# Kernel tuning notes

Hardware: AMD Instinct MI355X
Metric: run time of the kernel (lower is better)

Reference implementation:

```python
import jax, jax.numpy as jnp
import numpy as np

N, E = 50000, 800000
IN_DIM, HIDDEN, LATENT = 128, 256, 64


def setup_inputs() -> dict:
    key = jax.random.key(0)
    ks = jax.random.split(key, 10)
    def lin(k, fan_in, fan_out):
        s = 1.0 / np.sqrt(fan_in)
        return jax.random.uniform(k, (fan_in, fan_out), jnp.float32, -s, s)
    x = jax.random.normal(ks[0], (N, IN_DIM), jnp.float32)
    edge_index = jax.random.randint(ks[1], (2, E), 0, N, jnp.int64)
    return {
        "x": x,
        "edge_index": edge_index,
        # enc1: SAGEConv(in_dim, hidden): lin_l (neighbors, with bias), lin_r (root, no bias)
        "W1l": lin(ks[2], IN_DIM, HIDDEN),
        "b1": jnp.zeros((HIDDEN,), jnp.float32),
        "W1r": lin(ks[3], IN_DIM, HIDDEN),
        # enc2: SAGEConv(hidden, latent)
        "W2l": lin(ks[4], HIDDEN, LATENT),
        "b2": jnp.zeros((LATENT,), jnp.float32),
        "W2r": lin(ks[5], HIDDEN, LATENT),
        # decoder Linear(latent, in_dim)
        "Wd": lin(ks[6], LATENT, IN_DIM),
        "bd": jax.random.uniform(ks[7], (IN_DIM,), jnp.float32, -1.0 / np.sqrt(LATENT), 1.0 / np.sqrt(LATENT)),
    }


def _sage_conv(x, src, dst, Wl, b, Wr, num_nodes):
    # PyG SAGEConv (aggr='mean'): out = lin_l(mean_{j in N(i)} x_j) + lin_r(x_i)
    summed = jax.ops.segment_sum(x[src], dst, num_segments=num_nodes)   # [N, d]
    cnt = jax.ops.segment_sum(jnp.ones((src.shape[0],), x.dtype), dst, num_segments=num_nodes)
    mean = summed / jnp.maximum(cnt, 1.0)[:, None]
    return mean @ Wl + b + x @ Wr


def reference(x, edge_index, W1l, b1, W1r, W2l, b2, W2r, Wd, bd):
    src, dst = edge_index[0], edge_index[1]
    n = x.shape[0]
    h = jax.nn.relu(_sage_conv(x, src, dst, W1l, b1, W1r, n))
    z = _sage_conv(h, src, dst, W2l, b2, W2r, n)
    x_hat = z @ Wd + bd
    return (z, x_hat)
```

## Files before the change

kernel.cpp:

```cpp
#include <hip/hip_runtime.h>
#include <stdint.h>

#define NN 50000
#define NE 800000
#define NB 196
#define NBK 196
#define NBUK 196
#define CHK 4096
#define MTOT (NBUK * NBK)
#define MSB 151
#define CVTB 6250
#define PREPB 418

typedef __bf16 bf16x8 __attribute__((ext_vector_type(8)));
typedef float f32x4 __attribute__((ext_vector_type(4)));
typedef unsigned short ushort_t;

__device__ inline float bf2f(uint16_t u) {
    union { uint32_t i; float f; } v; v.i = ((uint32_t)u) << 16; return v.f;
}
__device__ inline uint16_t f2bf(float f) {
    uint32_t u = __float_as_uint(f);
    u += 0x7fffu + ((u >> 16) & 1u);
    return (uint16_t)(u >> 16);
}
__device__ inline float rdf(const void* p, int i, int bf) {
    return bf ? bf2f(((const ushort_t*)p)[i]) : ((const float*)p)[i];
}

__device__ inline int blk_or(int v, int* flag) {
    if (threadIdx.x == 0) *flag = 0;
    __syncthreads();
    if (v) atomicOr(flag, 1);
    __syncthreads();
    return *flag;
}
__device__ inline int detect_sh(const int* __restrict__ ei, int* flag) {
    int t = threadIdx.x;
    int v = ei[2 * t + 1] | ei[2 * (t + 256) + 1] | ei[2 * (t + 512) + 1] | ei[2 * (t + 768) + 1];
    return blk_or(v, flag) ? 0 : 1;
}
__device__ inline int detect_bf(const ushort_t* __restrict__ xw, int* flag) {
    int t = threadIdx.x;
    int bad = 0;
#pragma unroll
    for (int r = 0; r < 2; ++r) {
        uint16_t w = xw[t + 256 * r];
        int e = (w >> 7) & 0xFF;
        if (!(w == 0 || (e >= 96 && e <= 144))) bad = 1;
    }
    return blk_or(bad, flag) ? 0 : 1;
}

__global__ __launch_bounds__(256) void k_stage1(const int* __restrict__ ei, const void* __restrict__ x,
                                                const void* __restrict__ W1l, const void* __restrict__ W1r,
                                                const void* __restrict__ W2l, const void* __restrict__ W2r,
                                                const void* __restrict__ Wd,
                                                const void* __restrict__ b1, const void* __restrict__ b2,
                                                const void* __restrict__ bd,
                                                int* __restrict__ cntm, ushort_t* __restrict__ xb,
                                                ushort_t* __restrict__ wt, ushort_t* __restrict__ w2lt,
                                                ushort_t* __restrict__ w2rt, ushort_t* __restrict__ wdt,
                                                float* __restrict__ b1f, float* __restrict__ b2f,
                                                float* __restrict__ bdf) {
    __shared__ int flag;
    int b = blockIdx.x, t = threadIdx.x;
    if (b < NBK) {
        int sh = detect_sh(ei, &flag);
        __shared__ int hist[NBUK];
        if (t < NBUK) hist[t] = 0;
        __syncthreads();
        for (int i = t; i < CHK; i += 256) {
            int e = b * CHK + i;
            if (e < NE) {
                int d = ei[(size_t)(NE + e) << sh];
                atomicAdd(&hist[d >> 8], 1);
            }
        }
        __syncthreads();
        if (t < NBUK) cntm[t * NBK + b] = hist[t];
    } else if (b < NBK + CVTB) {
        int bf = detect_bf((const ushort_t*)x, &flag);
        int i = (b - NBK) * 256 + t;
        if (bf) {
            reinterpret_cast<ushort4*>(xb)[i] = reinterpret_cast<const ushort4*>(x)[i];
        } else {
            float4 v = reinterpret_cast<const float4*>(x)[i];
            ushort4 o;
            o.x = f2bf(v.x); o.y = f2bf(v.y); o.z = f2bf(v.z); o.w = f2bf(v.w);
            reinterpret_cast<ushort4*>(xb)[i] = o;
        }
    } else {
        int bf = detect_bf((const ushort_t*)x, &flag);
        int idx = (b - NBK - CVTB) * 256 + t;
        if (idx < 65536) {
            int c = idx >> 8, k = idx & 255;
            float v = (k < 128) ? rdf(W1l, k * 256 + c, bf) : rdf(W1r, (k - 128) * 256 + c, bf);
            wt[c * 256 + k] = f2bf(v);
        } else if (idx < 81920) {
            int t2 = idx - 65536;
            int c = t2 >> 8, k = t2 & 255;
            w2lt[c * 256 + k] = f2bf(rdf(W2l, k * 64 + c, bf));
        } else if (idx < 98304) {
            int t2 = idx - 81920;
            int c = t2 >> 8, k = t2 & 255;
            w2rt[c * 256 + k] = f2bf(rdf(W2r, k * 64 + c, bf));
        } else if (idx < 106496) {
            int t2 = idx - 98304;
            int c = t2 >> 6, k = t2 & 63;
            wdt[c * 64 + k] = f2bf(rdf(Wd, k * 128 + c, bf));
        } else if (idx < 106752) {
            b1f[idx - 106496] = rdf(b1, idx - 106496, bf);
        } else if (idx < 106816) {
            b2f[idx - 106752] = rdf(b2, idx - 106752, bf);
        } else if (idx < 106944) {
            bdf[idx - 106816] = rdf(bd, idx - 106816, bf);
        }
    }
}

__device__ inline int block_scan256(int v, int* ws, int* btot) {
    int lane = threadIdx.x & 63, wv = threadIdx.x >> 6;
    int incl = v;
#pragma unroll
    for (int d = 1; d < 64; d <<= 1) {
        int n = __shfl_up(incl, d);
        if (lane >= d) incl += n;
    }
    if (lane == 63) ws[wv] = incl;
    __syncthreads();
    if (threadIdx.x == 0) {
        int r = 0;
#pragma unroll
        for (int k = 0; k < 4; ++k) { int t = ws[k]; ws[k] = r; r += t; }
        *btot = r;
    }
    __syncthreads();
    return ws[wv] + incl - v;
}

__global__ __launch_bounds__(256) void k_scanMA(const int* __restrict__ cntm, int* __restrict__ offm,
                                                int* __restrict__ bsM) {
    __shared__ int ws[4]; __shared__ int btot;
    int i = blockIdx.x * 256 + threadIdx.x;
    int v = (i < MTOT) ? cntm[i] : 0;
    int excl = block_scan256(v, ws, &btot);
    if (i < MTOT) offm[i] = excl;
    if (threadIdx.x == 0) bsM[blockIdx.x] = btot;
}

__device__ inline void bsm_prefix(const int* __restrict__ bsM, int* bsPre, int* ws, int* btot) {
    int t = threadIdx.x;
    int v = (t < MSB) ? bsM[t] : 0;
    int excl = block_scan256(v, ws, &btot[0]);
    bsPre[t] = excl;
    __syncthreads();
}

__global__ __launch_bounds__(256) void k_scatterC(const int* __restrict__ ei,
                                                  const int* __restrict__ offm, const int* __restrict__ bsM,
                                                  uint32_t* __restrict__ pairs) {
    __shared__ int cur[NBUK];
    __shared__ int bsPre[256];
    __shared__ int ws[4]; __shared__ int btot;
    __shared__ int flag;
    int t = threadIdx.x, blk = blockIdx.x;
    int sh = detect_sh(ei, &flag);
    bsm_prefix(bsM, bsPre, ws, &btot);
    if (t < NBUK) {
        int g = t * NBK + blk;
        cur[t] = offm[g] + bsPre[g >> 8];
    }
    __syncthreads();
    for (int i = t; i < CHK; i += 256) {
        int e = blk * CHK + i;
        if (e < NE) {
            int s = ei[(size_t)e << sh];
            int d = ei[(size_t)(NE + e) << sh];
            int pos = atomicAdd(&cur[d >> 8], 1);
            pairs[pos] = (uint32_t)s | ((uint32_t)(d & 255) << 16);
        }
    }
}

__global__ __launch_bounds__(256) void k_d12(const uint32_t* __restrict__ pairs, const int* __restrict__ offm,
                                             const int* __restrict__ bsM,
                                             int* __restrict__ rowptr, ushort_t* __restrict__ srclist) {
    __shared__ int hist[256];
    __shared__ int cur[256];
    __shared__ int bsPre[256];
    __shared__ int ws[4]; __shared__ int btot;
    int t = threadIdx.x, b = blockIdx.x;
    bsm_prefix(bsM, bsPre, ws, &btot);
    __shared__ int sbeg, send;
    if (t == 0) {
        int g0 = b * NBK;
        sbeg = offm[g0] + bsPre[g0 >> 8];
        if (b + 1 < NBUK) {
            int g1 = (b + 1) * NBK;
            send = offm[g1] + bsPre[g1 >> 8];
        } else {
            send = NE;
        }
    }
    hist[t] = 0;
    __syncthreads();
    int beg = sbeg, end = send;
    for (int i = beg + t; i < end; i += 256) {
        uint32_t p = pairs[i];
        atomicAdd(&hist[p >> 16], 1);
    }
    __syncthreads();
    int v = hist[t];
    int excl = block_scan256(v, ws, &btot);
    int node = b * 256 + t;
    int rp = beg + excl;
    if (node < NN) rowptr[node] = rp;
    cur[t] = rp;
    if (b == 0 && t == 0) rowptr[NN] = NE;
    __syncthreads();
    for (int i = beg + t; i < end; i += 256) {
        uint32_t p = pairs[i];
        int pos = atomicAdd(&cur[p >> 16], 1);
        srclist[pos] = (ushort_t)(p & 0xffff);
    }
}

__global__ __launch_bounds__(256) void k_agg128(const ushort_t* __restrict__ xb, const int* __restrict__ rowptr,
                                                const ushort_t* __restrict__ srclist, ushort_t* __restrict__ out) {
    int node = (blockIdx.x * 256 + threadIdx.x) >> 6;
    int lane = threadIdx.x & 63;
    if (node >= NN) return;
    int half = lane >> 5, l32 = lane & 31;
    int beg = rowptr[node], end = rowptr[node + 1];
    float a0 = 0.f, a1 = 0.f, a2 = 0.f, a3 = 0.f;
    int j = beg + half;
    for (; j + 14 < end; j += 16) {
        ushort4 p[8];
#pragma unroll
        for (int u = 0; u < 8; ++u) {
            int s = srclist[j + 2 * u];
            p[u] = *reinterpret_cast<const ushort4*>(xb + (size_t)s * 128 + l32 * 4);
        }
#pragma unroll
        for (int u = 0; u < 8; ++u) {
            a0 += bf2f(p[u].x); a1 += bf2f(p[u].y); a2 += bf2f(p[u].z); a3 += bf2f(p[u].w);
        }
    }
    for (; j + 6 < end; j += 8) {
        ushort4 p[4];
#pragma unroll
        for (int u = 0; u < 4; ++u) {
            int s = srclist[j + 2 * u];
            p[u] = *reinterpret_cast<const ushort4*>(xb + (size_t)s * 128 + l32 * 4);
        }
#pragma unroll
        for (int u = 0; u < 4; ++u) {
            a0 += bf2f(p[u].x); a1 += bf2f(p[u].y); a2 += bf2f(p[u].z); a3 += bf2f(p[u].w);
        }
    }
    for (; j < end; j += 2) {
        int s = srclist[j];
        ushort4 p = *reinterpret_cast<const ushort4*>(xb + (size_t)s * 128 + l32 * 4);
        a0 += bf2f(p.x); a1 += bf2f(p.y); a2 += bf2f(p.z); a3 += bf2f(p.w);
    }
    a0 += __shfl_xor(a0, 32);
    a1 += __shfl_xor(a1, 32);
    a2 += __shfl_xor(a2, 32);
    a3 += __shfl_xor(a3, 32);
    if (half == 0) {
        float inv = 1.0f / (float)max(end - beg, 1);
        ushort4 o;
        o.x = f2bf(a0 * inv); o.y = f2bf(a1 * inv); o.z = f2bf(a2 * inv); o.w = f2bf(a3 * inv);
        *reinterpret_cast<ushort4*>(out + (size_t)node * 128 + l32 * 4) = o;
    }
}

__global__ __launch_bounds__(256, 2) void k_gemm12(const ushort_t* __restrict__ meanx, const ushort_t* __restrict__ xb,
                                                   const ushort_t* __restrict__ wt, const float* __restrict__ b1f,
                                                   const ushort_t* __restrict__ w2lt, const ushort_t* __restrict__ w2rt,
                                                   const float* __restrict__ b2f,
                                                   ushort_t* __restrict__ y, float* __restrict__ r) {
    __shared__ alignas(16) ushort_t ht[16 * 256];
    int wv = threadIdx.x >> 6, lane = threadIdx.x & 63;
    int m = lane & 15, q = lane >> 4;
    bf16x8 B1[8][4];
#pragma unroll
    for (int ks = 0; ks < 8; ++ks) {
        int kb = ks * 32 + q * 8;
#pragma unroll
        for (int ct = 0; ct < 4; ++ct)
            B1[ks][ct] = *reinterpret_cast<const bf16x8*>(wt + (size_t)(wv * 64 + ct * 16 + m) * 256 + kb);
    }
    int op = wv >> 1;
    int cb = (wv & 1) * 32;
    const ushort_t* wtx = op ? w2rt : w2lt;
    bf16x8 B2[8][2];
#pragma unroll
    for (int ks = 0; ks < 8; ++ks) {
        int kb = ks * 32 + q * 8;
#pragma unroll
        for (int ct = 0; ct < 2; ++ct)
            B2[ks][ct] = *reinterpret_cast<const bf16x8*>(wtx + (size_t)(cb + ct * 16 + m) * 256 + kb);
    }
    float bias2[2];
#pragma unroll
    for (int ct = 0; ct < 2; ++ct) bias2[ct] = b2f[cb + ct * 16 + m];

    const int ntiles = NN / 16;
    for (int t = blockIdx.x; t < ntiles; t += gridDim.x) {
        int r0 = t * 16;
        int row = r0 + m;
        f32x4 acc[4];
#pragma unroll
        for (int ct = 0; ct < 4; ++ct) acc[ct] = (f32x4){0.f, 0.f, 0.f, 0.f};
#pragma unroll
        for (int ks = 0; ks < 8; ++ks) {
            int kb = ks * 32 + q * 8;
            const ushort_t* ap = (ks < 4) ? (meanx + (size_t)row * 128 + kb)
                                          : (xb + (size_t)row * 128 + (kb - 128));
            bf16x8 a = *reinterpret_cast<const bf16x8*>(ap);
#pragma unroll
            for (int ct = 0; ct < 4; ++ct)
                acc[ct] = __builtin_amdgcn_mfma_f32_16x16x32_bf16(a, B1[ks][ct], acc[ct], 0, 0, 0);
        }
#pragma unroll
        for (int ct = 0; ct < 4; ++ct) {
            int c = wv * 64 + ct * 16 + m;
            float bias = b1f[c];
#pragma unroll
            for (int i = 0; i < 4; ++i) {
                int lr = q * 4 + i;
                int off = (lr * 512 + c * 2) ^ ((lr & 7) << 4);
                *reinterpret_cast<ushort_t*>(reinterpret_cast<char*>(ht) + off) =
                    f2bf(fmaxf(acc[ct][i] + bias, 0.f));
            }
        }
        __syncthreads();
        f32x4 acc2[2];
        acc2[0] = (f32x4){0.f, 0.f, 0.f, 0.f}; acc2[1] = acc2[0];
#pragma unroll
        for (int ks = 0; ks < 8; ++ks) {
            int boff = (m * 512 + ks * 64 + q * 16) ^ ((m & 7) << 4);
            bf16x8 a = *reinterpret_cast<const bf16x8*>(reinterpret_cast<const char*>(ht) + boff);
#pragma unroll
            for (int ct = 0; ct < 2; ++ct)
                acc2[ct] = __builtin_amdgcn_mfma_f32_16x16x32_bf16(a, B2[ks][ct], acc2[ct], 0, 0, 0);
        }
#pragma unroll
        for (int ct = 0; ct < 2; ++ct) {
            int c = cb + ct * 16 + m;
#pragma unroll
            for (int i = 0; i < 4; ++i) {
                int rr = r0 + q * 4 + i;
                if (op == 0) y[(size_t)rr * 64 + c] = f2bf(acc2[ct][i]);
                else         r[(size_t)rr * 64 + c] = acc2[ct][i] + bias2[ct];
            }
        }
        __syncthreads();
    }
}

__global__ __launch_bounds__(256) void k_agg2g3(const ushort_t* __restrict__ y, const int* __restrict__ rowptr,
                                                const ushort_t* __restrict__ srclist,
                                                float* zr,
                                                const ushort_t* __restrict__ wdt, const float* __restrict__ bdf,
                                                float* __restrict__ xhat) {
    __shared__ alignas(16) ushort_t zt[16][72];
    int b = blockIdx.x;
    int wv = threadIdx.x >> 6, lane = threadIdx.x & 63;
    int m = lane & 15, q = lane >> 4;
    bf16x8 B[2][2];
#pragma unroll
    for (int ks = 0; ks < 2; ++ks) {
        int kb = ks * 32 + q * 8;
#pragma unroll
        for (int ct = 0; ct < 2; ++ct)
            B[ks][ct] = *reinterpret_cast<const bf16x8*>(wdt + (size_t)(wv * 32 + ct * 16 + m) * 64 + kb);
    }
    float bias0 = bdf[wv * 32 + m], bias1 = bdf[wv * 32 + 16 + m];

    int quarter = lane >> 4, l16 = lane & 15;
#pragma unroll
    for (int s = 0; s < 4; ++s) {
        int node = b * 16 + wv * 4 + s;
        int beg = rowptr[node], end = rowptr[node + 1];
        float a0 = 0.f, a1 = 0.f, a2 = 0.f, a3 = 0.f;
        int j = beg + quarter;
        for (; j + 12 < end; j += 16) {
            ushort4 p[4];
#pragma unroll
            for (int u = 0; u < 4; ++u) {
                int sx = srclist[j + 4 * u];
                p[u] = *reinterpret_cast<const ushort4*>(y + (size_t)sx * 64 + l16 * 4);
            }
#pragma unroll
            for (int u = 0; u < 4; ++u) {
                a0 += bf2f(p[u].x); a1 += bf2f(p[u].y); a2 += bf2f(p[u].z); a3 += bf2f(p[u].w);
            }
        }
        for (; j < end; j += 4) {
            int sx = srclist[j];
            ushort4 p = *reinterpret_cast<const ushort4*>(y + (size_t)sx * 64 + l16 * 4);
            a0 += bf2f(p.x); a1 += bf2f(p.y); a2 += bf2f(p.z); a3 += bf2f(p.w);
        }
        a0 += __shfl_xor(a0, 16); a0 += __shfl_xor(a0, 32);
        a1 += __shfl_xor(a1, 16); a1 += __shfl_xor(a1, 32);
        a2 += __shfl_xor(a2, 16); a2 += __shfl_xor(a2, 32);
        a3 += __shfl_xor(a3, 16); a3 += __shfl_xor(a3, 32);
        if (quarter == 0) {
            float inv = 1.0f / (float)max(end - beg, 1);
            float4 rv = *reinterpret_cast<const float4*>(zr + (size_t)node * 64 + l16 * 4);
            float z0 = a0 * inv + rv.x;
            float z1 = a1 * inv + rv.y;
            float z2 = a2 * inv + rv.z;
            float z3 = a3 * inv + rv.w;
            float4 zo; zo.x = z0; zo.y = z1; zo.z = z2; zo.w = z3;
            *reinterpret_cast<float4*>(zr + (size_t)node * 64 + l16 * 4) = zo;
            uint2 o;
            o.x = (uint32_t)f2bf(z0) | ((uint32_t)f2bf(z1) << 16);
            o.y = (uint32_t)f2bf(z2) | ((uint32_t)f2bf(z3) << 16);
            *reinterpret_cast<uint2*>(&zt[wv * 4 + s][l16 * 4]) = o;
        }
    }
    __syncthreads();
    f32x4 acc[2];
    acc[0] = (f32x4){0.f, 0.f, 0.f, 0.f}; acc[1] = acc[0];
#pragma unroll
    for (int ks = 0; ks < 2; ++ks) {
        bf16x8 a = *reinterpret_cast<const bf16x8*>(&zt[m][ks * 32 + q * 8]);
#pragma unroll
        for (int ct = 0; ct < 2; ++ct)
            acc[ct] = __builtin_amdgcn_mfma_f32_16x16x32_bf16(a, B[ks][ct], acc[ct], 0, 0, 0);
    }
#pragma unroll
    for (int ct = 0; ct < 2; ++ct) {
        int c = wv * 32 + ct * 16 + m;
        float bb = ct ? bias1 : bias0;
#pragma unroll
        for (int i = 0; i < 4; ++i) {
            int rr = b * 16 + q * 4 + i;
            xhat[(size_t)rr * 128 + c] = acc[ct][i] + bb;
        }
    }
}

extern "C" void kernel_launch(void* const* d_in, const int* in_sizes, int n_in,
                              void* d_out, int out_size, void* d_ws, size_t ws_size,
                              hipStream_t stream) {
    const void *px = nullptr, *pei = nullptr, *pW1l = nullptr, *pW1r = nullptr,
               *pW2l = nullptr, *pW2r = nullptr, *pWd = nullptr,
               *pb1 = nullptr, *pb2 = nullptr, *pbd = nullptr;
    for (int i = 0; i < n_in; ++i) {
        const void* p = d_in[i];
        switch (in_sizes[i]) {
            case 6400000: px  = p; break;
            case 1600000: pei = p; break;
            case 32768:   if (!pW1l) pW1l = p; else pW1r = p; break;
            case 16384:   if (!pW2l) pW2l = p; else pW2r = p; break;
            case 8192:    pWd = p; break;
            case 256:     pb1 = p; break;
            case 128:     pbd = p; break;
            case 64:      pb2 = p; break;
            default: break;
        }
    }
    if (!px || !pei || !pW1l || !pW1r || !pW2l || !pW2r || !pWd || !pb1 || !pb2 || !pbd) {
        px = d_in[0]; pei = d_in[1]; pW1l = d_in[2]; pb1 = d_in[3]; pW1r = d_in[4];
        pW2l = d_in[5]; pb2 = d_in[6]; pW2r = d_in[7]; pWd = d_in[8]; pbd = d_in[9];
    }
    const int* ei = (const int*)pei;

    char* base = (char*)d_ws;
    size_t off = 0;
    auto alloc = [&](size_t bytes) -> void* {
        void* r = base + off;
        off = (off + bytes + 255) & ~(size_t)255;
        return r;
    };
    int* rowptr   = (int*)alloc((size_t)(NN + 1) * 4);
    int* cntm     = (int*)alloc((size_t)MTOT * 4);
    int* offm     = (int*)alloc((size_t)MTOT * 4);
    int* bsM      = (int*)alloc(256 * 4);
    uint32_t* pairs = (uint32_t*)alloc((size_t)NE * 4);
    ushort_t* srclist = (ushort_t*)alloc((size_t)NE * 2);
    ushort_t* wt   = (ushort_t*)alloc((size_t)65536 * 2);
    ushort_t* w2lt = (ushort_t*)alloc((size_t)16384 * 2);
    ushort_t* w2rt = (ushort_t*)alloc((size_t)16384 * 2);
    ushort_t* wdt  = (ushort_t*)alloc((size_t)8192 * 2);
    float* b1f    = (float*)alloc(256 * 4);
    float* b2f    = (float*)alloc(64 * 4);
    float* bdf    = (float*)alloc(128 * 4);
    ushort_t* xb  = (ushort_t*)alloc((size_t)NN * 128 * 2);
    ushort_t* y   = (ushort_t*)alloc((size_t)NN * 64 * 2);

    float* out_z    = (float*)d_out;
    float* out_xhat = out_z + (size_t)NN * 64;

    ushort_t* meanx = (ushort_t*)out_xhat;
    float*    rbuf  = out_z;

    k_stage1<<<NBK + CVTB + PREPB, 256, 0, stream>>>(ei, px, pW1l, pW1r, pW2l, pW2r, pWd, pb1, pb2, pbd,
                                                     cntm, xb, wt, w2lt, w2rt, wdt, b1f, b2f, bdf);

    k_scanMA<<<MSB, 256, 0, stream>>>(cntm, offm, bsM);
    k_scatterC<<<NBK, 256, 0, stream>>>(ei, offm, bsM, pairs);
    k_d12<<<NBUK, 256, 0, stream>>>(pairs, offm, bsM, rowptr, srclist);

    int ab = (NN + 3) / 4;
    k_agg128<<<ab, 256, 0, stream>>>(xb, rowptr, srclist, meanx);

    k_gemm12<<<512, 256, 0, stream>>>(meanx, xb, wt, b1f, w2lt, w2rt, b2f, y, rbuf);
    k_agg2g3<<<NN / 16, 256, 0, stream>>>(y, rowptr, srclist, rbuf, wdt, bdf, out_xhat);
}
```

Measured before the change: 222.4 us.

## Fuse first-layer neighbor mean aggregation into the layer-1/2 GEMM kernel

```diff
diff --git a/kernel.cpp b/kernel.cpp
--- a/kernel.cpp
+++ b/kernel.cpp
@@ -226,62 +226,14 @@
     }
 }
 
-__global__ __launch_bounds__(256) void k_agg128(const ushort_t* __restrict__ xb, const int* __restrict__ rowptr,
-                                                const ushort_t* __restrict__ srclist, ushort_t* __restrict__ out) {
-    int node = (blockIdx.x * 256 + threadIdx.x) >> 6;
-    int lane = threadIdx.x & 63;
-    if (node >= NN) return;
-    int half = lane >> 5, l32 = lane & 31;
-    int beg = rowptr[node], end = rowptr[node + 1];
-    float a0 = 0.f, a1 = 0.f, a2 = 0.f, a3 = 0.f;
-    int j = beg + half;
-    for (; j + 14 < end; j += 16) {
-        ushort4 p[8];
-#pragma unroll
-        for (int u = 0; u < 8; ++u) {
-            int s = srclist[j + 2 * u];
-            p[u] = *reinterpret_cast<const ushort4*>(xb + (size_t)s * 128 + l32 * 4);
-        }
-#pragma unroll
-        for (int u = 0; u < 8; ++u) {
-            a0 += bf2f(p[u].x); a1 += bf2f(p[u].y); a2 += bf2f(p[u].z); a3 += bf2f(p[u].w);
-        }
-    }
-    for (; j + 6 < end; j += 8) {
-        ushort4 p[4];
-#pragma unroll
-        for (int u = 0; u < 4; ++u) {
-            int s = srclist[j + 2 * u];
-            p[u] = *reinterpret_cast<const ushort4*>(xb + (size_t)s * 128 + l32 * 4);
-        }
-#pragma unroll
-        for (int u = 0; u < 4; ++u) {
-            a0 += bf2f(p[u].x); a1 += bf2f(p[u].y); a2 += bf2f(p[u].z); a3 += bf2f(p[u].w);
-        }
-    }
-    for (; j < end; j += 2) {
-        int s = srclist[j];
-        ushort4 p = *reinterpret_cast<const ushort4*>(xb + (size_t)s * 128 + l32 * 4);
-        a0 += bf2f(p.x); a1 += bf2f(p.y); a2 += bf2f(p.z); a3 += bf2f(p.w);
-    }
-    a0 += __shfl_xor(a0, 32);
-    a1 += __shfl_xor(a1, 32);
-    a2 += __shfl_xor(a2, 32);
-    a3 += __shfl_xor(a3, 32);
-    if (half == 0) {
-        float inv = 1.0f / (float)max(end - beg, 1);
-        ushort4 o;
-        o.x = f2bf(a0 * inv); o.y = f2bf(a1 * inv); o.z = f2bf(a2 * inv); o.w = f2bf(a3 * inv);
-        *reinterpret_cast<ushort4*>(out + (size_t)node * 128 + l32 * 4) = o;
-    }
-}
-
-__global__ __launch_bounds__(256, 2) void k_gemm12(const ushort_t* __restrict__ meanx, const ushort_t* __restrict__ xb,
-                                                   const ushort_t* __restrict__ wt, const float* __restrict__ b1f,
-                                                   const ushort_t* __restrict__ w2lt, const ushort_t* __restrict__ w2rt,
-                                                   const float* __restrict__ b2f,
-                                                   ushort_t* __restrict__ y, float* __restrict__ r) {
+__global__ __launch_bounds__(256, 2) void k_ag12(const ushort_t* __restrict__ xb, const int* __restrict__ rowptr,
+                                                 const ushort_t* __restrict__ srclist,
+                                                 const ushort_t* __restrict__ wt, const float* __restrict__ b1f,
+                                                 const ushort_t* __restrict__ w2lt, const ushort_t* __restrict__ w2rt,
+                                                 const float* __restrict__ b2f,
+                                                 ushort_t* __restrict__ y, float* __restrict__ r) {
     __shared__ alignas(16) ushort_t ht[16 * 256];
+    __shared__ alignas(16) ushort_t xt[16 * 128];
     int wv = threadIdx.x >> 6, lane = threadIdx.x & 63;
     int m = lane & 15, q = lane >> 4;
     bf16x8 B1[8][4];
@@ -307,9 +259,48 @@
 #pragma unroll
     for (int ct = 0; ct < 2; ++ct) bias2[ct] = b2f[cb + ct * 16 + m];
 
+    int half = lane >> 5, l32 = lane & 31;
     const int ntiles = NN / 16;
     for (int t = blockIdx.x; t < ntiles; t += gridDim.x) {
         int r0 = t * 16;
+#pragma unroll
+        for (int s = 0; s < 4; ++s) {
+            int node = r0 + wv * 4 + s;
+            int beg = rowptr[node], end = rowptr[node + 1];
+            float a0 = 0.f, a1 = 0.f, a2 = 0.f, a3 = 0.f;
+            int j = beg + half;
+            for (; j + 6 < end; j += 8) {
+                ushort4 p[4];
+#pragma unroll
+                for (int u = 0; u < 4; ++u) {
+                    int sx = srclist[j + 2 * u];
+                    p[u] = *reinterpret_cast<const ushort4*>(xb + (size_t)sx * 128 + l32 * 4);
+                }
+#pragma unroll
+                for (int u = 0; u < 4; ++u) {
+                    a0 += bf2f(p[u].x); a1 += bf2f(p[u].y); a2 += bf2f(p[u].z); a3 += bf2f(p[u].w);
+                }
+            }
+            for (; j < end; j += 2) {
+                int sx = srclist[j];
+                ushort4 p = *reinterpret_cast<const ushort4*>(xb + (size_t)sx * 128 + l32 * 4);
+                a0 += bf2f(p.x); a1 += bf2f(p.y); a2 += bf2f(p.z); a3 += bf2f(p.w);
+            }
+            a0 += __shfl_xor(a0, 32);
+            a1 += __shfl_xor(a1, 32);
+            a2 += __shfl_xor(a2, 32);
+            a3 += __shfl_xor(a3, 32);
+            if (half == 0) {
+                float inv = 1.0f / (float)max(end - beg, 1);
+                int nl = wv * 4 + s;
+                uint2 o;
+                o.x = (uint32_t)f2bf(a0 * inv) | ((uint32_t)f2bf(a1 * inv) << 16);
+                o.y = (uint32_t)f2bf(a2 * inv) | ((uint32_t)f2bf(a3 * inv) << 16);
+                int off = (nl * 256 + l32 * 8) ^ ((nl & 7) << 4);
+                *reinterpret_cast<uint2*>(reinterpret_cast<char*>(xt) + off) = o;
+            }
+        }
+        __syncthreads();
         int row = r0 + m;
         f32x4 acc[4];
 #pragma unroll
@@ -317,9 +308,13 @@
 #pragma unroll
         for (int ks = 0; ks < 8; ++ks) {
             int kb = ks * 32 + q * 8;
-            const ushort_t* ap = (ks < 4) ? (meanx + (size_t)row * 128 + kb)
-                                          : (xb + (size_t)row * 128 + (kb - 128));
-            bf16x8 a = *reinterpret_cast<const bf16x8*>(ap);
+            bf16x8 a;
+            if (ks < 4) {
+                int boff = (m * 256 + kb * 2) ^ ((m & 7) << 4);
+                a = *reinterpret_cast<const bf16x8*>(reinterpret_cast<const char*>(xt) + boff);
+            } else {
+                a = *reinterpret_cast<const bf16x8*>(xb + (size_t)row * 128 + (kb - 128));
+            }
 #pragma unroll
             for (int ct = 0; ct < 4; ++ct)
                 acc[ct] = __builtin_amdgcn_mfma_f32_16x16x32_bf16(a, B1[ks][ct], acc[ct], 0, 0, 0);
@@ -497,8 +492,7 @@
     float* out_z    = (float*)d_out;
     float* out_xhat = out_z + (size_t)NN * 64;
 
-    ushort_t* meanx = (ushort_t*)out_xhat;
-    float*    rbuf  = out_z;
+    float* rbuf = out_z;
 
     k_stage1<<<NBK + CVTB + PREPB, 256, 0, stream>>>(ei, px, pW1l, pW1r, pW2l, pW2r, pWd, pb1, pb2, pbd,
                                                      cntm, xb, wt, w2lt, w2rt, wdt, b1f, b2f, bdf);
@@ -507,9 +501,6 @@
     k_scatterC<<<NBK, 256, 0, stream>>>(ei, offm, bsM, pairs);
     k_d12<<<NBUK, 256, 0, stream>>>(pairs, offm, bsM, rowptr, srclist);
 
-    int ab = (NN + 3) / 4;
-    k_agg128<<<ab, 256, 0, stream>>>(xb, rowptr, srclist, meanx);
-
-    k_gemm12<<<512, 256, 0, stream>>>(meanx, xb, wt, b1f, w2lt, w2rt, b2f, y, rbuf);
+    k_ag12<<<512, 256, 0, stream>>>(xb, rowptr, srclist, wt, b1f, w2lt, w2rt, b2f, y, rbuf);
     k_agg2g3<<<NN / 16, 256, 0, stream>>>(y, rowptr, srclist, rbuf, wdt, bdf, out_xhat);
 }
```

Measured after the change: 321.6 us. 1.45x slower.
